# Kernel tuning notes

Measured on AMD Instinct MI355X. Metric: run time of the kernel, lower is better.

Reference implementation:

```python
import jax, jax.numpy as jnp
import numpy as np

NUM_NEG_PAIRS = 64
NUM_NEG_INDICES_FOR_LOSS = 16
B, C, H, W = 1, 64, 768, 768
HW = H * W


def setup_inputs() -> dict:
    key = jax.random.key(0)
    k1, k2, k3, k4 = jax.random.split(key, 4)
    feats1 = jax.random.normal(k1, (B, C, H, W), dtype=jnp.float32)
    feats2 = jax.random.normal(k2, (B, C, H, W), dtype=jnp.float32)
    positive_pairs = jax.random.randint(k3, (64, 2), 0, HW, dtype=jnp.int64 if jax.config.jax_enable_x64 else jnp.int32)
    negative_indices = jax.random.randint(k4, (NUM_NEG_PAIRS,), 0, HW, dtype=jnp.int64 if jax.config.jax_enable_x64 else jnp.int32)
    return {"feats1": feats1, "feats2": feats2,
            "positive_pairs": positive_pairs,
            "negative_indices": negative_indices}


def reference(feats1, feats2, positive_pairs, negative_indices):
    # feats1/feats2: [1, C, H, W] -> flatten to [C, HW] (matches .view(C, -1) with B=1)
    f1 = feats1.reshape(C, -1)
    f2 = feats2.reshape(C, -1)
    sel = f1[:, negative_indices]                      # [C, P]
    # squared L2 distance of each selected feature vs all HW locations of feats2
    # ||a-b||^2 = ||a||^2 + ||b||^2 - 2 a.b  (ReLU as in original; dist is nonneg)
    d = (jnp.sum(sel * sel, axis=0)[:, None]
         + jnp.sum(f2 * f2, axis=0)[None, :]
         - 2.0 * jnp.einsum('cp,cn->pn', sel, f2))     # [P, HW]
    d = jax.nn.relu(d)
    # NOTE: the original's mask-exclusion check compares FLOAT distance values
    # against an INT index mask (`dist[...].item() in mask`), which is never true
    # for continuous features, so the effective math is: take the K smallest
    # distances per negative, negate, and average.
    smallest = -jax.lax.top_k(-d, NUM_NEG_INDICES_FOR_LOSS)[0]   # [P, K] smallest dists
    negative_loss = jnp.mean(-smallest, axis=1)                   # [P]
    return jnp.mean(negative_loss)
```

## Files before the change

kernel.cpp:

```cpp
#include <hip/hip_runtime.h>
#include <cstdint>

#define CD 64
#define HWD 589824
#define K1_GRID 1152
#define T_PER 4
#define K1_ROWS (K1_GRID * 4)
#define FMAXV 3.402823466e+38f

#define AS1 __attribute__((address_space(1)))
#define AS3 __attribute__((address_space(3)))

typedef float f32x16 __attribute__((ext_vector_type(16)));
typedef short bf16x8 __attribute__((ext_vector_type(8)));

__device__ __forceinline__ short f2bf(float f) {
    unsigned u = __float_as_uint(f);
    u = u + 0x7FFFu + ((u >> 16) & 1u);
    return (short)(u >> 16);
}

__device__ __forceinline__ void ins4(float4& t, float x) {
    if (x < t.w) {
        if (x < t.z) { t.w = t.z;
            if (x < t.y) { t.z = t.y;
                if (x < t.x) { t.y = t.x; t.x = x; } else t.y = x;
            } else t.z = x;
        } else t.w = x;
    }
}

__global__ __launch_bounds__(64) void kA_pack(
    const float* __restrict__ f1, const int* __restrict__ nidx,
    short* __restrict__ sel_bf, float* __restrict__ sel2,
    unsigned* __restrict__ ticket)
{
    const int p = blockIdx.x, k = threadIdx.x;
    if (p == 0 && k == 0) *ticket = 0u;
    float v = f1[(long)k * HWD + nidx[p]];
    float s = v * v;
#pragma unroll
    for (int off = 32; off; off >>= 1) s += __shfl_xor(s, off);
    sel_bf[p * CD + k] = f2bf(v);
    if (k == 0) sel2[p] = s;
}

__global__ __launch_bounds__(256, 4) void k1_topk(
    const float* __restrict__ f2, const short* __restrict__ sel_bf,
    const float* __restrict__ sel2, float4* __restrict__ cells)
{
    __shared__ float lds[4][CD][32];
    const int tid = threadIdx.x;
    const int lane = tid & 63, wid = tid >> 6;
    const int l31 = lane & 31, lh = lane >> 5;
    const int gw = blockIdx.x * 4 + wid;
    const long nb = (long)gw * (T_PER * 32);

    bf16x8 sf0[4], sf1[4];
#pragma unroll
    for (int ks = 0; ks < 4; ++ks) {
        sf0[ks] = *(const bf16x8*)(sel_bf + l31 * CD + 16 * ks + 8 * lh);
        sf1[ks] = *(const bf16x8*)(sel_bf + (l31 + 32) * CD + 16 * ks + 8 * lh);
    }
    const float sel20 = sel2[l31], sel21 = sel2[l31 + 32];

    const int srow = lane >> 3;
    const int scol = (lane & 7) * 4;

    float4 t = make_float4(FMAXV, FMAXV, FMAXV, FMAXV);
    float4 u = t;

#pragma unroll
    for (int tt = 0; tt < T_PER; ++tt) {
        const long n0 = nb + (long)tt * 32;

#pragma unroll
        for (int kk = 0; kk < 8; ++kk) {
            const float* gp = f2 + (long)(8 * kk + srow) * HWD + n0 + scol;
            __builtin_amdgcn_global_load_lds((const AS1 void*)gp,
                                             (AS3 void*)&lds[wid][8 * kk][0], 16, 0, 0);
        }
        asm volatile("s_waitcnt vmcnt(0)" ::: "memory");
        __builtin_amdgcn_sched_barrier(0);

        float fs = 0.f;
        f32x16 a0, a1;
#pragma unroll
        for (int i = 0; i < 16; ++i) { a0[i] = 0.f; a1[i] = 0.f; }
#pragma unroll
        for (int ks = 0; ks < 4; ++ks) {
            bf16x8 af;
#pragma unroll
            for (int j = 0; j < 8; ++j) {
                float v = lds[wid][16 * ks + 8 * lh + j][l31];
                fs += v * v;
                af[j] = f2bf(v);
            }
            a0 = __builtin_amdgcn_mfma_f32_32x32x16_bf16(af, sf0[ks], a0, 0, 0, 0);
            a1 = __builtin_amdgcn_mfma_f32_32x32x16_bf16(af, sf1[ks], a1, 0, 0, 0);
        }
        fs += __shfl_xor(fs, 32);

#pragma unroll
        for (int i = 0; i < 16; ++i) {
            int r = (i & 3) + 8 * (i >> 2) + 4 * lh;
            float fr2 = __shfl(fs, r);
            ins4(t, fmaxf(sel20 + fr2 - 2.f * a0[i], 0.f));
            ins4(u, fmaxf(sel21 + fr2 - 2.f * a1[i], 0.f));
        }
        asm volatile("s_waitcnt lgkmcnt(0)" ::: "memory");
        __builtin_amdgcn_sched_barrier(0);
    }

    {
        float4 o;
        o.x = __shfl_xor(t.x, 32); o.y = __shfl_xor(t.y, 32);
        o.z = __shfl_xor(t.z, 32); o.w = __shfl_xor(t.w, 32);
        ins4(t, o.x); ins4(t, o.y); ins4(t, o.z); ins4(t, o.w);
        o.x = __shfl_xor(u.x, 32); o.y = __shfl_xor(u.y, 32);
        o.z = __shfl_xor(u.z, 32); o.w = __shfl_xor(u.w, 32);
        ins4(u, o.x); ins4(u, o.y); ins4(u, o.z); ins4(u, o.w);
    }
    if (lh == 0) {
        cells[(long)gw * CD + l31]      = t;
        cells[(long)gw * CD + l31 + 32] = u;
    }
}

__global__ __launch_bounds__(1024) void k2_sel(
    const float4* __restrict__ cells, float* __restrict__ partial,
    unsigned* __restrict__ ticket, float* __restrict__ out)
{
    const int p = blockIdx.x;
    const int tid = threadIdx.x;
    const int lane = tid & 63, wid = tid >> 6;
    __shared__ unsigned long long wmin[16];

    float4 b0 = cells[(long)(tid)        * CD + p];
    float4 b1 = cells[(long)(tid + 1024) * CD + p];
    float4 b2 = cells[(long)(tid + 2048) * CD + p];
    float4 b3 = cells[(long)(tid + 3072) * CD + p];
    float4 b4 = (tid < K1_ROWS - 4096)
                ? cells[(long)(tid + 4096) * CD + p]
                : make_float4(FMAXV, FMAXV, FMAXV, FMAXV);

    float4 t = make_float4(FMAXV, FMAXV, FMAXV, FMAXV);
    ins4(t, b0.x); ins4(t, b0.y); ins4(t, b0.z); ins4(t, b0.w);
    ins4(t, b1.x); ins4(t, b1.y); ins4(t, b1.z); ins4(t, b1.w);
    ins4(t, b2.x); ins4(t, b2.y); ins4(t, b2.z); ins4(t, b2.w);
    ins4(t, b3.x); ins4(t, b3.y); ins4(t, b3.z); ins4(t, b3.w);
    ins4(t, b4.x); ins4(t, b4.y); ins4(t, b4.z); ins4(t, b4.w);

    float sum = 0.f;
    for (int rd = 0; rd < 16; ++rd) {
        unsigned long long key =
            ((unsigned long long)__float_as_uint(t.x) << 32) | (unsigned)tid;
#pragma unroll
        for (int off = 32; off; off >>= 1) {
            unsigned long long o = __shfl_xor(key, off);
            if (o < key) key = o;
        }
        if (lane == 0) wmin[wid] = key;
        __syncthreads();
        unsigned long long gk = wmin[0];
#pragma unroll
        for (int w = 1; w < 16; ++w) if (wmin[w] < gk) gk = wmin[w];
        sum += __uint_as_float((unsigned)(gk >> 32));
        if ((unsigned)(gk & 0xFFFFFFFFu) == (unsigned)tid) {
            t.x = t.y; t.y = t.z; t.z = t.w; t.w = FMAXV;
        }
        __syncthreads();
    }

    if (tid == 0) {
        partial[p] = sum;
        __threadfence();
        unsigned tk = atomicAdd(ticket, 1u);
        if (tk == CD - 1) {
            __threadfence();
            float s = 0.f;
            const volatile float* vp = partial;
            for (int q = 0; q < CD; ++q) s += vp[q];
            out[0] = -s / 1024.0f;
        }
    }
}

extern "C" void kernel_launch(void* const* d_in, const int* in_sizes, int n_in,
                              void* d_out, int out_size, void* d_ws, size_t ws_size,
                              hipStream_t stream)
{
    const float* f1   = (const float*)d_in[0];
    const float* f2   = (const float*)d_in[1];
    const int*   nidx = (const int*)d_in[3];
    float* out = (float*)d_out;

    float4*   cells   = (float4*)d_ws;
    short*    sel_bf  = (short*)(cells + (long)K1_ROWS * CD);
    float*    sel2    = (float*)(sel_bf + CD * CD);
    float*    partial = sel2 + CD;
    unsigned* ticket  = (unsigned*)(partial + CD);

    kA_pack<<<CD,        64, 0, stream>>>(f1, nidx, sel_bf, sel2, ticket);
    k1_topk<<<K1_GRID,  256, 0, stream>>>(f2, sel_bf, sel2, cells);
    k2_sel <<<CD,      1024, 0, stream>>>(cells, partial, ticket, out);
}
```

Measured before the change: 84.18 us.

## Load feats2 tiles directly into registers instead of staging through LDS

Removes the global_load_lds staging buffer and explicit waitcnt barriers, so each lane reads its feature column straight from global memory (coalesced across 32 lanes per channel row) and converts it to bf16 for the MFMA. The grid changes from 1152 blocks with 4 tiles per wave to 1536 blocks with 3 tiles per wave, which gives more waves and no LDS limit on occupancy. The second-stage reduction loop is generalized to the new row count. The trade-off is less explicit control over load/compute overlap and narrower per-lane loads (scalar floats instead of 16-byte LDS DMA).

```diff
diff --git a/kernel.cpp b/kernel.cpp
--- a/kernel.cpp
+++ b/kernel.cpp
@@ -3,13 +3,11 @@
 
 #define CD 64
 #define HWD 589824
-#define K1_GRID 1152
-#define T_PER 4
-#define K1_ROWS (K1_GRID * 4)
+#define K1_BLOCKS 1536
+#define K1_WAVES (K1_BLOCKS * 4)
+#define TPW 3
+#define K1_ROWS K1_WAVES
 #define FMAXV 3.402823466e+38f
-
-#define AS1 __attribute__((address_space(1)))
-#define AS3 __attribute__((address_space(3)))
 
 typedef float f32x16 __attribute__((ext_vector_type(16)));
 typedef short bf16x8 __attribute__((ext_vector_type(8)));
@@ -30,6 +28,32 @@
     }
 }
 
+__device__ __forceinline__ void tile_dist(
+    const float* __restrict__ fp,
+    const bf16x8* __restrict__ sf0, const bf16x8* __restrict__ sf1,
+    int lh, f32x16& acc0, f32x16& acc1, float& fs)
+{
+    fs = 0.f;
+#pragma unroll
+    for (int i = 0; i < 16; ++i) { acc0[i] = 0.f; acc1[i] = 0.f; }
+#pragma unroll
+    for (int ks = 0; ks < 4; ++ks) {
+        float av[8];
+#pragma unroll
+        for (int j = 0; j < 8; ++j)
+            av[j] = fp[(long)(16 * ks + 8 * lh + j) * HWD];
+        bf16x8 af;
+#pragma unroll
+        for (int j = 0; j < 8; ++j) {
+            fs += av[j] * av[j];
+            af[j] = f2bf(av[j]);
+        }
+        acc0 = __builtin_amdgcn_mfma_f32_32x32x16_bf16(af, sf0[ks], acc0, 0, 0, 0);
+        acc1 = __builtin_amdgcn_mfma_f32_32x32x16_bf16(af, sf1[ks], acc1, 0, 0, 0);
+    }
+    fs += __shfl_xor(fs, 32);
+}
+
 __global__ __launch_bounds__(64) void kA_pack(
     const float* __restrict__ f1, const int* __restrict__ nidx,
     short* __restrict__ sel_bf, float* __restrict__ sel2,
@@ -45,16 +69,14 @@
     if (k == 0) sel2[p] = s;
 }
 
-__global__ __launch_bounds__(256, 4) void k1_topk(
+__global__ __launch_bounds__(256) void k1_topk(
     const float* __restrict__ f2, const short* __restrict__ sel_bf,
     const float* __restrict__ sel2, float4* __restrict__ cells)
 {
-    __shared__ float lds[4][CD][32];
     const int tid = threadIdx.x;
     const int lane = tid & 63, wid = tid >> 6;
     const int l31 = lane & 31, lh = lane >> 5;
     const int gw = blockIdx.x * 4 + wid;
-    const long nb = (long)gw * (T_PER * 32);
 
     bf16x8 sf0[4], sf1[4];
 #pragma unroll
@@ -64,42 +86,14 @@
     }
     const float sel20 = sel2[l31], sel21 = sel2[l31 + 32];
 
-    const int srow = lane >> 3;
-    const int scol = (lane & 7) * 4;
-
     float4 t = make_float4(FMAXV, FMAXV, FMAXV, FMAXV);
     float4 u = t;
 
 #pragma unroll
-    for (int tt = 0; tt < T_PER; ++tt) {
-        const long n0 = nb + (long)tt * 32;
-
-#pragma unroll
-        for (int kk = 0; kk < 8; ++kk) {
-            const float* gp = f2 + (long)(8 * kk + srow) * HWD + n0 + scol;
-            __builtin_amdgcn_global_load_lds((const AS1 void*)gp,
-                                             (AS3 void*)&lds[wid][8 * kk][0], 16, 0, 0);
-        }
-        asm volatile("s_waitcnt vmcnt(0)" ::: "memory");
-        __builtin_amdgcn_sched_barrier(0);
-
-        float fs = 0.f;
-        f32x16 a0, a1;
-#pragma unroll
-        for (int i = 0; i < 16; ++i) { a0[i] = 0.f; a1[i] = 0.f; }
-#pragma unroll
-        for (int ks = 0; ks < 4; ++ks) {
-            bf16x8 af;
-#pragma unroll
-            for (int j = 0; j < 8; ++j) {
-                float v = lds[wid][16 * ks + 8 * lh + j][l31];
-                fs += v * v;
-                af[j] = f2bf(v);
-            }
-            a0 = __builtin_amdgcn_mfma_f32_32x32x16_bf16(af, sf0[ks], a0, 0, 0, 0);
-            a1 = __builtin_amdgcn_mfma_f32_32x32x16_bf16(af, sf1[ks], a1, 0, 0, 0);
-        }
-        fs += __shfl_xor(fs, 32);
+    for (int tt = 0; tt < TPW; ++tt) {
+        const long n0 = (long)(gw * TPW + tt) * 32;
+        f32x16 a0, a1; float fs;
+        tile_dist(f2 + n0 + l31, sf0, sf1, lh, a0, a1, fs);
 
 #pragma unroll
         for (int i = 0; i < 16; ++i) {
@@ -108,8 +102,6 @@
             ins4(t, fmaxf(sel20 + fr2 - 2.f * a0[i], 0.f));
             ins4(u, fmaxf(sel21 + fr2 - 2.f * a1[i], 0.f));
         }
-        asm volatile("s_waitcnt lgkmcnt(0)" ::: "memory");
-        __builtin_amdgcn_sched_barrier(0);
     }
 
     {
@@ -136,20 +128,12 @@
     const int lane = tid & 63, wid = tid >> 6;
     __shared__ unsigned long long wmin[16];
 
-    float4 b0 = cells[(long)(tid)        * CD + p];
-    float4 b1 = cells[(long)(tid + 1024) * CD + p];
-    float4 b2 = cells[(long)(tid + 2048) * CD + p];
-    float4 b3 = cells[(long)(tid + 3072) * CD + p];
-    float4 b4 = (tid < K1_ROWS - 4096)
-                ? cells[(long)(tid + 4096) * CD + p]
-                : make_float4(FMAXV, FMAXV, FMAXV, FMAXV);
-
     float4 t = make_float4(FMAXV, FMAXV, FMAXV, FMAXV);
-    ins4(t, b0.x); ins4(t, b0.y); ins4(t, b0.z); ins4(t, b0.w);
-    ins4(t, b1.x); ins4(t, b1.y); ins4(t, b1.z); ins4(t, b1.w);
-    ins4(t, b2.x); ins4(t, b2.y); ins4(t, b2.z); ins4(t, b2.w);
-    ins4(t, b3.x); ins4(t, b3.y); ins4(t, b3.z); ins4(t, b3.w);
-    ins4(t, b4.x); ins4(t, b4.y); ins4(t, b4.z); ins4(t, b4.w);
+#pragma unroll
+    for (int q = 0; q < K1_ROWS / 1024; ++q) {
+        float4 b = cells[(long)(tid + q * 1024) * CD + p];
+        ins4(t, b.x); ins4(t, b.y); ins4(t, b.z); ins4(t, b.w);
+    }
 
     float sum = 0.f;
     for (int rd = 0; rd < 16; ++rd) {
@@ -201,7 +185,7 @@
     float*    partial = sel2 + CD;
     unsigned* ticket  = (unsigned*)(partial + CD);
 
-    kA_pack<<<CD,        64, 0, stream>>>(f1, nidx, sel_bf, sel2, ticket);
-    k1_topk<<<K1_GRID,  256, 0, stream>>>(f2, sel_bf, sel2, cells);
-    k2_sel <<<CD,      1024, 0, stream>>>(cells, partial, ticket, out);
+    kA_pack<<<CD,         64, 0, stream>>>(f1, nidx, sel_bf, sel2, ticket);
+    k1_topk<<<K1_BLOCKS, 256, 0, stream>>>(f2, sel_bf, sel2, cells);
+    k2_sel <<<CD,       1024, 0, stream>>>(cells, partial, ticket, out);
 }
```

New measurement: 85.67 us. About the same (+1.8%).
